# Performance work log

Hardware: AMD Instinct MI355X
Metric: run time of the kernel (lower is better)

Reference implementation:

```python
import jax, jax.numpy as jnp
import numpy as np


def squash(s):
    # s: (..., d); v = ||s|| / (1 + ||s||^2) * s
    norm = jnp.linalg.norm(s, axis=-1, keepdims=True)
    return norm / (1.0 + norm * norm) * s


def setup_inputs() -> dict:
    key = jax.random.key(0)
    k1, k2, k3 = jax.random.split(key, 3)
    batch, n_in, d_in, n_out, d_out = 256, 1152, 8, 10, 16
    u_i = jax.random.normal(k1, (batch, n_in, d_in), dtype=jnp.float32)
    weight = jax.random.normal(k2, (1, n_in, n_out, d_in, d_out), dtype=jnp.float32)
    bias = jax.random.normal(k3, (n_in, n_out, 1), dtype=jnp.float32)
    return {"u_i": u_i, "weight": weight, "bias": bias, "r": 3}


def reference(u_i, weight, bias, r):
    batch, n_in, d_in = u_i.shape
    # predictions u_j|i: (batch, n_in, n_out, d_out)
    u_ji = jnp.einsum('bnd,node->bnoe', u_i, weight[0]) + bias  # bias (n_in,n_out,1) broadcasts over d_out
    # dynamic routing
    b = jnp.zeros(u_ji.shape[:3], dtype=u_ji.dtype)  # (batch, n_in, n_out)
    v = None
    for _ in range(r):  # r is a small static iteration count
        c = jax.nn.softmax(b, axis=-1)                      # over n_out
        s = jnp.einsum('bno,bnoe->boe', c, u_ji)            # weighted sum over n_in
        v = squash(s)                                       # (batch, n_out, d_out)
        b = b + jnp.einsum('bnoe,boe->bno', u_ji, v)        # agreement update
    return v
```

## Files before the change

### kernel.cpp

```cpp
#include <hip/hip_runtime.h>


#define B    256
#define N    1152
#define NO   10
#define DI   8
#define DE   16
#define NTILE   9
#define NTILES  128
#define BPT     2
#define BG      128
#define BGS     2
#define THREADS 640

#define SP_OFF 0
#define SP_SZ  (NTILES * B * NO * DE)
#define VS_OFF (SP_OFF + SP_SZ)
#define VS_SZ  (B * NO * DE)
#define UT_OFF (VS_OFF + VS_SZ)
#define UT_SZ  (2 * N * B * 4)

__global__ __launch_bounds__(256)
void transpose_kernel(const float* __restrict__ u, float* __restrict__ ut) {
    const int lane = threadIdx.x & 63;
    const int wv   = threadIdx.x >> 6;
    const int n    = blockIdx.x * 4 + wv;
    const int b    = blockIdx.y * 64 + lane;
    const float* up = u + ((size_t)b * N + n) * DI;
    const float4 a0 = *(const float4*)up;
    const float4 a1 = *(const float4*)(up + 4);
    *(float4*)(ut + ((size_t)(n * 2 + 0) * B + b) * 4) = a0;
    *(float4*)(ut + ((size_t)(n * 2 + 1) * B + b) * 4) = a1;
}

__global__ __launch_bounds__(THREADS, 3)
void routing_kernel(const float* __restrict__ u,
                    const float* __restrict__ ut,
                    const float* __restrict__ w,
                    const float* __restrict__ bias,
                    const float* __restrict__ vsum,
                    float* __restrict__ s_part,
                    const int has_v,
                    const int use_ut) {
    __shared__ float lgx[2][NO][BG];
    const int tid  = threadIdx.x;
    const int lane = tid & 63;
    const int wv   = __builtin_amdgcn_readfirstlane(tid >> 6);
    const int o    = wv;

    const int id   = blockIdx.x;
    const int xcd  = id & 7;
    const int s    = id >> 3;
    const int g    = s >> 4;
    const int t    = ((s & 15) << 3) | xcd;
    const int n0   = t * NTILE;
    const int bb   = g * BG;

    float bvs[NTILE];
#pragma unroll
    for (int i = 0; i < NTILE; ++i)
        bvs[i] = bias[(n0 + i) * NO + o];

    float4 vv[BPT][4];
#pragma unroll
    for (int bi = 0; bi < BPT; ++bi)
#pragma unroll
        for (int eq = 0; eq < 4; ++eq)
            vv[bi][eq] = make_float4(0.f, 0.f, 0.f, 0.f);
    if (has_v) {
#pragma unroll
        for (int bi = 0; bi < BPT; ++bi)
#pragma unroll
            for (int eq = 0; eq < 4; ++eq)
                vv[bi][eq] = *(const float4*)(vsum +
                    ((size_t)(bb + bi * 64 + lane) * NO + o) * DE + eq * 4);
    }

    float4 acc[BPT][4];
#pragma unroll
    for (int bi = 0; bi < BPT; ++bi)
#pragma unroll
        for (int eq = 0; eq < 4; ++eq)
            acc[bi][eq] = make_float4(0.f, 0.f, 0.f, 0.f);

    for (int i = 0; i < NTILE; ++i) {
        const int n = n0 + i;

        float ur[BPT][DI];
#pragma unroll
        for (int bi = 0; bi < BPT; ++bi) {
            const int b = bb + bi * 64 + lane;
            float4 u0, u1;
            if (use_ut) {
                const float* up = ut + ((size_t)(n * 2) * B + b) * 4;
                u0 = *(const float4*)up;
                u1 = *(const float4*)(up + B * 4);
            } else {
                const float* up = u + ((size_t)b * N + n) * DI;
                u0 = *(const float4*)up;
                u1 = *(const float4*)(up + 4);
            }
            ur[bi][0] = u0.x; ur[bi][1] = u0.y; ur[bi][2] = u0.z; ur[bi][3] = u0.w;
            ur[bi][4] = u1.x; ur[bi][5] = u1.y; ur[bi][6] = u1.z; ur[bi][7] = u1.w;
        }

        const float* wp = w + ((size_t)n * NO + o) * (DI * DE);
        const float bv = bvs[i];
        float4 uji[BPT][4];
#pragma unroll
        for (int bi = 0; bi < BPT; ++bi)
#pragma unroll
            for (int eq = 0; eq < 4; ++eq)
                uji[bi][eq] = make_float4(bv, bv, bv, bv);
#pragma unroll
        for (int d = 0; d < DI; ++d) {
#pragma unroll
            for (int eq = 0; eq < 4; ++eq) {
                const float4 w4 = *(const float4*)(wp + d * DE + eq * 4);
#pragma unroll
                for (int bi = 0; bi < BPT; ++bi) {
                    uji[bi][eq].x += ur[bi][d] * w4.x;
                    uji[bi][eq].y += ur[bi][d] * w4.y;
                    uji[bi][eq].z += ur[bi][d] * w4.z;
                    uji[bi][eq].w += ur[bi][d] * w4.w;
                }
            }
        }

        float c[BPT];
        if (has_v) {
            const int pb = i & 1;
#pragma unroll
            for (int bi = 0; bi < BPT; ++bi) {
                float lg = 0.f;
#pragma unroll
                for (int eq = 0; eq < 4; ++eq)
                    lg += uji[bi][eq].x * vv[bi][eq].x + uji[bi][eq].y * vv[bi][eq].y
                        + uji[bi][eq].z * vv[bi][eq].z + uji[bi][eq].w * vv[bi][eq].w;
                lgx[pb][o][bi * 64 + lane] = lg;
            }
            __syncthreads();
#pragma unroll
            for (int bi = 0; bi < BPT; ++bi) {
                float l[NO];
#pragma unroll
                for (int oo = 0; oo < NO; ++oo) l[oo] = lgx[pb][oo][bi * 64 + lane];
                float m = l[0];
#pragma unroll
                for (int oo = 1; oo < NO; ++oo) m = fmaxf(m, l[oo]);
                float sum = 0.f;
#pragma unroll
                for (int oo = 0; oo < NO; ++oo) { l[oo] = __expf(l[oo] - m); sum += l[oo]; }
                c[bi] = l[o] / sum;
            }
        } else {
            c[0] = 0.1f; c[1] = 0.1f;
        }

#pragma unroll
        for (int bi = 0; bi < BPT; ++bi)
#pragma unroll
            for (int eq = 0; eq < 4; ++eq) {
                acc[bi][eq].x += c[bi] * uji[bi][eq].x;
                acc[bi][eq].y += c[bi] * uji[bi][eq].y;
                acc[bi][eq].z += c[bi] * uji[bi][eq].z;
                acc[bi][eq].w += c[bi] * uji[bi][eq].w;
            }
    }

#pragma unroll
    for (int bi = 0; bi < BPT; ++bi) {
        float* sp = s_part + (((size_t)t * B + bb + bi * 64 + lane) * NO + o) * DE;
#pragma unroll
        for (int eq = 0; eq < 4; ++eq)
            *(float4*)(sp + eq * 4) = acc[bi][eq];
    }
}

__global__ __launch_bounds__(256)
void squash_kernel(const float* __restrict__ s_part,
                   float* __restrict__ vsum,
                   float* __restrict__ out,
                   const int accum) {
    const int t0 = blockIdx.x * 256 + threadIdx.x;
    const int q  = t0 & 3;
    const int g  = t0 >> 2;

    float s = 0.f;
    const float* sp = s_part + (size_t)(q * 32) * (B * NO * DE) + g;
#pragma unroll 8
    for (int i = 0; i < 32; ++i)
        s += sp[(size_t)i * (B * NO * DE)];
    s += __shfl_xor(s, 1);
    s += __shfl_xor(s, 2);

    float nsq = s * s;
#pragma unroll
    for (int msk = 4; msk <= 32; msk <<= 1) nsq += __shfl_xor(nsq, msk);
    const float nrm   = sqrtf(nsq);
    const float scale = nrm / (1.f + nsq);
    const float val   = s * scale;

    if (q == 0) {
        out[g]  = val;
        vsum[g] = accum ? (vsum[g] + val) : val;
    }
}

extern "C" void kernel_launch(void* const* d_in, const int* in_sizes, int n_in,
                              void* d_out, int out_size, void* d_ws, size_t ws_size,
                              hipStream_t stream) {
    const float* u    = (const float*)d_in[0];
    const float* w    = (const float*)d_in[1];
    const float* bias = (const float*)d_in[2];

    float* wsf    = (float*)d_ws;
    float* s_part = wsf + SP_OFF;
    float* vsum   = wsf + VS_OFF;
    float* ut     = wsf + UT_OFF;
    float* out    = (float*)d_out;

    const int use_ut = (ws_size >= (size_t)(SP_SZ + VS_SZ + UT_SZ) * sizeof(float));

    if (use_ut)
        transpose_kernel<<<dim3(N / 4, B / 64), 256, 0, stream>>>(u, ut);

    for (int it = 0; it < 3; ++it) {
        routing_kernel<<<NTILES * BGS, THREADS, 0, stream>>>(
            u, ut, w, bias, vsum, s_part, it > 0, use_ut);
        squash_kernel<<<(4 * B * NO * DE) / 256, 256, 0, stream>>>(
            s_part, vsum, out, it > 0);
    }
}
```

Before: 181.7 us.

## Materialize predicted capsule vectors once and reuse across routing iterations

Adds a first-pass kernel that computes u_ji = u·W + bias, writes it to a workspace buffer in a batch-contiguous layout, and accumulates the uniform-coupling first iteration. Two later-pass kernels read u_ji back and skip the recomputation of the small matmul. This trades recompute FLOPs for a very large buffer of roughly 190 MB, written once and read twice. The new path only runs when the workspace is big enough; otherwise the old fused recompute path is used.

```diff
diff --git a/kernel.cpp b/kernel.cpp
--- a/kernel.cpp
+++ b/kernel.cpp
@@ -12,6 +12,7 @@
 #define BG      128
 #define BGS     2
 #define THREADS 640
+#define GRID    (NTILES * BGS)
 
 #define SP_OFF 0
 #define SP_SZ  (NTILES * B * NO * DE)
@@ -19,6 +20,8 @@
 #define VS_SZ  (B * NO * DE)
 #define UT_OFF (VS_OFF + VS_SZ)
 #define UT_SZ  (2 * N * B * 4)
+#define UJ_OFF (UT_OFF + UT_SZ)
+#define UJ_SZ  ((size_t)N * NO * 4 * B * 4)
 
 __global__ __launch_bounds__(256)
 void transpose_kernel(const float* __restrict__ u, float* __restrict__ ut) {
@@ -31,6 +34,186 @@
     const float4 a1 = *(const float4*)(up + 4);
     *(float4*)(ut + ((size_t)(n * 2 + 0) * B + b) * 4) = a0;
     *(float4*)(ut + ((size_t)(n * 2 + 1) * B + b) * 4) = a1;
+}
+
+#define DECODE_ID()                                        \
+    const int xcd  = id & 7;                               \
+    const int sg   = id >> 3;                              \
+    const int g    = sg >> 4;                              \
+    const int t    = ((sg & 15) << 3) | xcd;               \
+    const int n0   = t * NTILE;                            \
+    const int bb   = g * BG;
+
+__global__ __launch_bounds__(THREADS, 3)
+void phase1_kernel(const float* __restrict__ ut,
+                   const float* __restrict__ w,
+                   const float* __restrict__ bias,
+                   float* __restrict__ s_part,
+                   float* __restrict__ uj) {
+    const int tid  = threadIdx.x;
+    const int lane = tid & 63;
+    const int wv   = __builtin_amdgcn_readfirstlane(tid >> 6);
+    const int o    = wv;
+    const int id   = blockIdx.x;
+    DECODE_ID();
+
+    float bvs[NTILE];
+#pragma unroll
+    for (int i = 0; i < NTILE; ++i)
+        bvs[i] = bias[(n0 + i) * NO + o];
+
+    float4 acc[BPT][4];
+#pragma unroll
+    for (int bi = 0; bi < BPT; ++bi)
+#pragma unroll
+        for (int eq = 0; eq < 4; ++eq)
+            acc[bi][eq] = make_float4(0.f, 0.f, 0.f, 0.f);
+
+    for (int i = 0; i < NTILE; ++i) {
+        const int n = n0 + i;
+
+        float ur[BPT][DI];
+#pragma unroll
+        for (int bi = 0; bi < BPT; ++bi) {
+            const int b = bb + bi * 64 + lane;
+            const float* up = ut + ((size_t)(n * 2) * B + b) * 4;
+            const float4 u0 = *(const float4*)up;
+            const float4 u1 = *(const float4*)(up + B * 4);
+            ur[bi][0] = u0.x; ur[bi][1] = u0.y; ur[bi][2] = u0.z; ur[bi][3] = u0.w;
+            ur[bi][4] = u1.x; ur[bi][5] = u1.y; ur[bi][6] = u1.z; ur[bi][7] = u1.w;
+        }
+
+        const float* wp = w + ((size_t)n * NO + o) * (DI * DE);
+        const float bv = bvs[i];
+        float4 uji[BPT][4];
+#pragma unroll
+        for (int bi = 0; bi < BPT; ++bi)
+#pragma unroll
+            for (int eq = 0; eq < 4; ++eq)
+                uji[bi][eq] = make_float4(bv, bv, bv, bv);
+#pragma unroll
+        for (int d = 0; d < DI; ++d) {
+#pragma unroll
+            for (int eq = 0; eq < 4; ++eq) {
+                const float4 w4 = *(const float4*)(wp + d * DE + eq * 4);
+#pragma unroll
+                for (int bi = 0; bi < BPT; ++bi) {
+                    uji[bi][eq].x += ur[bi][d] * w4.x;
+                    uji[bi][eq].y += ur[bi][d] * w4.y;
+                    uji[bi][eq].z += ur[bi][d] * w4.z;
+                    uji[bi][eq].w += ur[bi][d] * w4.w;
+                }
+            }
+        }
+
+#pragma unroll
+        for (int bi = 0; bi < BPT; ++bi) {
+            const int b = bb + bi * 64 + lane;
+#pragma unroll
+            for (int eq = 0; eq < 4; ++eq) {
+                *(float4*)(uj + ((((size_t)n * NO + o) * 4 + eq) * B + b) * 4)
+                    = uji[bi][eq];
+                acc[bi][eq].x += 0.1f * uji[bi][eq].x;
+                acc[bi][eq].y += 0.1f * uji[bi][eq].y;
+                acc[bi][eq].z += 0.1f * uji[bi][eq].z;
+                acc[bi][eq].w += 0.1f * uji[bi][eq].w;
+            }
+        }
+    }
+
+#pragma unroll
+    for (int bi = 0; bi < BPT; ++bi) {
+        float* sp = s_part + (((size_t)t * B + bb + bi * 64 + lane) * NO + o) * DE;
+#pragma unroll
+        for (int eq = 0; eq < 4; ++eq)
+            *(float4*)(sp + eq * 4) = acc[bi][eq];
+    }
+}
+
+__global__ __launch_bounds__(THREADS, 3)
+void phase2_kernel(const float* __restrict__ uj,
+                   const float* __restrict__ vsum,
+                   float* __restrict__ s_part) {
+    __shared__ float lgx[2][NO][BG];
+    const int tid  = threadIdx.x;
+    const int lane = tid & 63;
+    const int wv   = __builtin_amdgcn_readfirstlane(tid >> 6);
+    const int o    = wv;
+    const int id   = blockIdx.x;
+    DECODE_ID();
+
+    float4 vv[BPT][4];
+#pragma unroll
+    for (int bi = 0; bi < BPT; ++bi)
+#pragma unroll
+        for (int eq = 0; eq < 4; ++eq)
+            vv[bi][eq] = *(const float4*)(vsum +
+                ((size_t)(bb + bi * 64 + lane) * NO + o) * DE + eq * 4);
+
+    float4 acc[BPT][4];
+#pragma unroll
+    for (int bi = 0; bi < BPT; ++bi)
+#pragma unroll
+        for (int eq = 0; eq < 4; ++eq)
+            acc[bi][eq] = make_float4(0.f, 0.f, 0.f, 0.f);
+
+    for (int i = 0; i < NTILE; ++i) {
+        const int n = n0 + i;
+
+        float4 uji[BPT][4];
+#pragma unroll
+        for (int bi = 0; bi < BPT; ++bi) {
+            const int b = bb + bi * 64 + lane;
+#pragma unroll
+            for (int eq = 0; eq < 4; ++eq)
+                uji[bi][eq] = *(const float4*)(uj +
+                    ((((size_t)n * NO + o) * 4 + eq) * B + b) * 4);
+        }
+
+        const int pb = i & 1;
+#pragma unroll
+        for (int bi = 0; bi < BPT; ++bi) {
+            float lg = 0.f;
+#pragma unroll
+            for (int eq = 0; eq < 4; ++eq)
+                lg += uji[bi][eq].x * vv[bi][eq].x + uji[bi][eq].y * vv[bi][eq].y
+                    + uji[bi][eq].z * vv[bi][eq].z + uji[bi][eq].w * vv[bi][eq].w;
+            lgx[pb][o][bi * 64 + lane] = lg;
+        }
+        __syncthreads();
+        float c[BPT];
+#pragma unroll
+        for (int bi = 0; bi < BPT; ++bi) {
+            float l[NO];
+#pragma unroll
+            for (int oo = 0; oo < NO; ++oo) l[oo] = lgx[pb][oo][bi * 64 + lane];
+            float m = l[0];
+#pragma unroll
+            for (int oo = 1; oo < NO; ++oo) m = fmaxf(m, l[oo]);
+            float sum = 0.f;
+#pragma unroll
+            for (int oo = 0; oo < NO; ++oo) { l[oo] = __expf(l[oo] - m); sum += l[oo]; }
+            c[bi] = l[o] / sum;
+        }
+
+#pragma unroll
+        for (int bi = 0; bi < BPT; ++bi)
+#pragma unroll
+            for (int eq = 0; eq < 4; ++eq) {
+                acc[bi][eq].x += c[bi] * uji[bi][eq].x;
+                acc[bi][eq].y += c[bi] * uji[bi][eq].y;
+                acc[bi][eq].z += c[bi] * uji[bi][eq].z;
+                acc[bi][eq].w += c[bi] * uji[bi][eq].w;
+            }
+    }
+
+#pragma unroll
+    for (int bi = 0; bi < BPT; ++bi) {
+        float* sp = s_part + (((size_t)t * B + bb + bi * 64 + lane) * NO + o) * DE;
+#pragma unroll
+        for (int eq = 0; eq < 4; ++eq)
+            *(float4*)(sp + eq * 4) = acc[bi][eq];
+    }
 }
 
 __global__ __launch_bounds__(THREADS, 3)
@@ -47,14 +230,8 @@
     const int lane = tid & 63;
     const int wv   = __builtin_amdgcn_readfirstlane(tid >> 6);
     const int o    = wv;
-
     const int id   = blockIdx.x;
-    const int xcd  = id & 7;
-    const int s    = id >> 3;
-    const int g    = s >> 4;
-    const int t    = ((s & 15) << 3) | xcd;
-    const int n0   = t * NTILE;
-    const int bb   = g * BG;
+    DECODE_ID();
 
     float bvs[NTILE];
 #pragma unroll
@@ -85,7 +262,6 @@
 
     for (int i = 0; i < NTILE; ++i) {
         const int n = n0 + i;
-
         float ur[BPT][DI];
 #pragma unroll
         for (int bi = 0; bi < BPT; ++bi) {
@@ -218,17 +394,31 @@
     float* s_part = wsf + SP_OFF;
     float* vsum   = wsf + VS_OFF;
     float* ut     = wsf + UT_OFF;
+    float* uj     = wsf + UJ_OFF;
     float* out    = (float*)d_out;
 
+    const size_t need_uj = ((size_t)UJ_OFF + UJ_SZ) * sizeof(float);
+    const int use_uj = (ws_size >= need_uj);
     const int use_ut = (ws_size >= (size_t)(SP_SZ + VS_SZ + UT_SZ) * sizeof(float));
 
-    if (use_ut)
+    if (use_uj) {
         transpose_kernel<<<dim3(N / 4, B / 64), 256, 0, stream>>>(u, ut);
-
-    for (int it = 0; it < 3; ++it) {
-        routing_kernel<<<NTILES * BGS, THREADS, 0, stream>>>(
-            u, ut, w, bias, vsum, s_part, it > 0, use_ut);
+        phase1_kernel<<<GRID, THREADS, 0, stream>>>(ut, w, bias, s_part, uj);
         squash_kernel<<<(4 * B * NO * DE) / 256, 256, 0, stream>>>(
-            s_part, vsum, out, it > 0);
-    }
-}
+            s_part, vsum, out, 0);
+        for (int it = 1; it < 3; ++it) {
+            phase2_kernel<<<GRID, THREADS, 0, stream>>>(uj, vsum, s_part);
+            squash_kernel<<<(4 * B * NO * DE) / 256, 256, 0, stream>>>(
+                s_part, vsum, out, 1);
+        }
+    } else {
+        if (use_ut)
+            transpose_kernel<<<dim3(N / 4, B / 64), 256, 0, stream>>>(u, ut);
+        for (int it = 0; it < 3; ++it) {
+            routing_kernel<<<GRID, THREADS, 0, stream>>>(
+                u, ut, w, bias, vsum, s_part, it > 0, use_ut);
+            squash_kernel<<<(4 * B * NO * DE) / 256, 256, 0, stream>>>(
+                s_part, vsum, out, it > 0);
+        }
+    }
+}
```

After: 201.6 us. 10.9% more time.
